# Optimization experiments

Measured on AMD Instinct MI355X. Metric: run time of the kernel, lower is better.

Reference implementation:

```python
import jax, jax.numpy as jnp
import numpy as np

B, C, H, W = 8, 256, 128, 128
NH, WS = 8, 8
HD = C // NH
WNH, WNW = H // WS, W // WS


def _rel_pos_index():
    coords = np.stack(np.meshgrid(np.arange(WS), np.arange(WS), indexing='ij'))  # [2,ws,ws]
    flat = coords.reshape(2, -1)
    rel = (flat[:, :, None] - flat[:, None, :]).transpose(1, 2, 0)  # [ws^2,ws^2,2]
    rel[..., 0] += WS - 1
    rel[..., 1] += WS - 1
    rel[..., 0] *= 2 * WS - 1
    return jnp.asarray(rel.sum(-1))  # [ws^2,ws^2]


def grid_sample(img, grid):
    # Bilinear, padding_mode='zeros', align_corners=True. img [N,C,H,W], grid [N,Hg,Wg,2] (x,y in [-1,1])
    N, Ci, Hi, Wi = img.shape
    gx = (grid[..., 0] + 1.0) * 0.5 * (Wi - 1)
    gy = (grid[..., 1] + 1.0) * 0.5 * (Hi - 1)
    x0 = jnp.floor(gx)
    y0 = jnp.floor(gy)
    x0i = x0.astype(jnp.int32)
    y0i = y0.astype(jnp.int32)
    wx1 = gx - x0
    wx0 = 1.0 - wx1
    wy1 = gy - y0
    wy0 = 1.0 - wy1
    nb = jnp.arange(N)[:, None, None]

    def corner(yi, xi, wgt):
        valid = (yi >= 0) & (yi < Hi) & (xi >= 0) & (xi < Wi)
        yc = jnp.clip(yi, 0, Hi - 1)
        xc = jnp.clip(xi, 0, Wi - 1)
        val = img[nb, :, yc, xc]  # [N,Hg,Wg,C]
        return val * (wgt * valid)[..., None]

    out = (corner(y0i, x0i, wy0 * wx0) + corner(y0i, x0i + 1, wy0 * wx1)
           + corner(y0i + 1, x0i, wy1 * wx0) + corner(y0i + 1, x0i + 1, wy1 * wx1))
    return jnp.transpose(out, (0, 3, 1, 2))


def setup_inputs() -> dict:
    key = jax.random.key(0)
    ks = jax.random.split(key, 10)
    f = lambda k, s, sc=1.0: jax.random.normal(k, s, dtype=jnp.float32) * sc
    return {
        'x': f(ks[0], (B, C, H, W)),
        'qkv_w': f(ks[1], (3 * C, C), 0.02),
        'qkv_b': f(ks[2], (3 * C,), 0.02),
        'bias_w': f(ks[3], (2 * NH, C), 0.02),
        'bias_b': f(ks[4], (2 * NH,), 0.02),
        'scale_w': f(ks[5], (2 * NH, C), 0.02),
        'scale_b': f(ks[6], (2 * NH,), 0.02),
        'proj_w': f(ks[7], (C, C), 0.02),
        'proj_b': f(ks[8], (C,), 0.02),
        'rpb_table': f(ks[9], ((2 * WS - 1) ** 2, NH), 0.02),
    }


def reference(x, qkv_w, qkv_b, bias_w, bias_b, scale_w, scale_b, proj_w, proj_b, rpb_table):
    scale = HD ** -0.5
    N = B * NH
    # ---- deterministic base sampling coordinates (shift=0, no padding since H,W % WS == 0) ----
    lin_w = jnp.linspace(-1.0, 1.0, W)
    lin_h = jnp.linspace(-1.0, 1.0, H)
    winref_w = lin_w.reshape(WNW, WS).mean(-1)  # window centers along width
    winref_h = lin_h.reshape(WNH, WS).mean(-1)
    off_w = jnp.arange(WS) * 2.0 / (W - 1)
    off_w = off_w - off_w.mean()
    off_h = jnp.arange(WS) * 2.0 / (H - 1)
    off_h = off_h - off_h.mean()
    base_x = jnp.broadcast_to(winref_w[None, None, :, None] + off_w[None, None, None, :], (WNH, WS, WNW, WS))
    base_y = jnp.broadcast_to((winref_h[:, None] + off_h[None, :])[:, :, None, None], (WNH, WS, WNW, WS))
    # ---- predicted per-head per-window biases & scales ----
    xp = jax.nn.leaky_relu(x.reshape(B, C, WNH, WS, WNW, WS).mean((3, 5)))  # [B,C,WNH,WNW]
    biases = (jnp.einsum('oc,bchw->bohw', bias_w, xp) + bias_b[None, :, None, None]).reshape(N, 2, WNH, WNW)
    bx = biases[:, 0] / WNW  # sampling_biases[:,0] / (w // ws)
    by = biases[:, 1] / WNH
    scales = (jnp.einsum('oc,bchw->bohw', scale_w, xp) + scale_b[None, :, None, None]).reshape(N, 2, WNH, WNW)
    sx, sy = scales[:, 0], scales[:, 1]
    # final = base + local_offsets * scale + bias (broadcast [N,WNH,1,WNW,1] over window interior)
    cx = base_x[None] + off_w[None, None, None, None, :] * sx[:, :, None, :, None] + bx[:, :, None, :, None]
    cy = base_y[None] + off_h[None, None, :, None, None] * sy[:, :, None, :, None] + by[:, :, None, :, None]
    grid = jnp.stack([cx, cy], -1).reshape(N, H, W, 2)
    # ---- qkv via 1x1 conv ----
    qkv = (jnp.einsum('oc,bchw->bohw', qkv_w, x) + qkv_b[None, :, None, None]).reshape(B, 3, NH, HD, H, W)
    q = qkv[:, 0].reshape(N, HD, H, W)
    k = qkv[:, 1].reshape(N, HD, H, W)
    v = qkv[:, 2].reshape(N, HD, H, W)
    ksamp = grid_sample(k, grid)
    vsamp = grid_sample(v, grid)

    def win(t):  # [N,HD,H,W] -> [B, nWin, NH, WS*WS, HD]
        t = t.reshape(B, NH, HD, WNH, WS, WNW, WS)
        return jnp.transpose(t, (0, 3, 5, 1, 4, 6, 2)).reshape(B, WNH * WNW, NH, WS * WS, HD)

    qw, kw, vw = win(q), win(ksamp), win(vsamp)
    rpb = jnp.transpose(rpb_table[_rel_pos_index().reshape(-1)].reshape(WS * WS, WS * WS, NH), (2, 0, 1))
    attn = jnp.einsum('bwhqd,bwhkd->bwhqk', qw, kw) * scale + rpb[None, None]
    attn = jax.nn.softmax(attn, axis=-1)
    out = jnp.einsum('bwhqk,bwhkd->bwhqd', attn, vw)
    out = out.reshape(B, WNH, WNW, NH, WS, WS, HD)
    out = jnp.transpose(out, (0, 3, 6, 1, 4, 2, 5)).reshape(B, C, H, W)
    out = jnp.einsum('oc,bchw->bohw', proj_w, out) + proj_b[None, :, None, None]
    return out
```

## Files before the change

### kernel.cpp

```cpp
#include <hip/hip_runtime.h>
#include <hip/hip_fp16.h>

#define B_ 8
#define C_ 256
#define H_ 128
#define W_ 128
#define NH_ 8
#define WS_ 8
#define HD_ 32
#define WN_ 16
#define NWIN_ 256
#define HW_ 16384

typedef unsigned short ushort_t;
typedef unsigned int uint_t;
typedef __attribute__((ext_vector_type(8))) short short8;
typedef _Float16 __attribute__((ext_vector_type(8))) half8;
typedef __attribute__((ext_vector_type(4))) float f32x4;

__device__ __forceinline__ ushort_t bf16_rtn(float x) {
    uint_t u = __float_as_uint(x);
    return (ushort_t)((u + 0x7FFFu + ((u >> 16) & 1u)) >> 16);
}
__device__ __forceinline__ uint_t bfpack(float a, float b) {
    return (uint_t)bf16_rtn(a) | ((uint_t)bf16_rtn(b) << 16);
}
__device__ __forceinline__ uint_t h2pack(float a, float b) {
    __half2 h = __floats2half2_rn(a, b);
    return __builtin_bit_cast(uint_t, h);
}

__global__ __launch_bounds__(256) void wpack_kernel(const float* __restrict__ w,
                            ushort_t* __restrict__ wpk) {
    int u = blockIdx.x*256 + threadIdx.x;
    int lane = u & 63;
    int f    = (u >> 6) & 3;
    int kk   = (u >> 8) & 1;
    int ks   = (u >> 9) & 3;
    int wm   = (u >> 11) & 1;
    int oc   = u >> 12;
    int o = oc*128 + wm*64 + f*16 + (lane & 15);
    int c = ks*64 + kk*32 + (lane >> 4)*8;
    const float* src = w + (size_t)o*256 + c;
    float4 v0 = *(const float4*)src;
    float4 v1 = *(const float4*)(src + 4);
    uint4 Hv;
    Hv.x = h2pack(v0.x, v0.y); Hv.y = h2pack(v0.z, v0.w);
    Hv.z = h2pack(v1.x, v1.y); Hv.w = h2pack(v1.z, v1.w);
    ((uint4*)wpk)[u] = Hv;
}

__global__ __launch_bounds__(256) void wconv_kernel(const float* __restrict__ w,
                            ushort_t* __restrict__ wh, int n4) {
    int i = blockIdx.x*256 + threadIdx.x;
    if (i >= n4) return;
    float4 v = ((const float4*)w)[i];
    ((uint2*)wh)[i] = make_uint2(bfpack(v.x, v.y), bfpack(v.z, v.w));
}

__global__ __launch_bounds__(256) void rpb_expand_kernel(const float* __restrict__ rpb_table,
                            float* __restrict__ rpbT) {
    int nh = blockIdx.x;
    int t = threadIdx.x;
    #pragma unroll
    for (int rr = 0; rr < 16; ++rr) {
        int e = t*16 + rr;
        int kcol = e >> 6, qrow = e & 63;
        int yq = qrow >> 3, xq = qrow & 7, yk = kcol >> 3, xk = kcol & 7;
        int idx = (yq - yk + 7)*15 + (xq - xk + 7);
        rpbT[((size_t)nh*64 + kcol)*64 + qrow] = rpb_table[idx*8 + nh];
    }
}

__global__ __launch_bounds__(256) void pool2_kernel(const float* __restrict__ xpart, float* __restrict__ xp) {
    int bc = blockIdx.x;
    int t = threadIdx.x;
    int wy = t >> 4, wxg = t & 15;
    const float* src = xpart + (size_t)bc*2048;
    float s = 0.f;
    #pragma unroll
    for (int i = 0; i < 8; ++i) s += src[(wy*8+i)*16 + wxg];
    s *= (1.f/64.f);
    xp[(size_t)bc*256 + t] = s > 0.f ? s : 0.01f*s;
}

__global__ __launch_bounds__(256) void params_kernel(const float* __restrict__ xp,
                              const float* __restrict__ bias_w, const float* __restrict__ bias_b,
                              const float* __restrict__ scale_w, const float* __restrict__ scale_b,
                              float* __restrict__ params) {
    __shared__ float xs[256];
    int blk = blockIdx.x;
    int b = blk >> 8, win = blk & 255;
    int t = threadIdx.x;
    xs[t] = xp[((size_t)(b*256 + t))*256 + win];
    __syncthreads();
    if (t < 32) {
        int which = t >> 4;
        int o = t & 15;
        const float* Wm = which ? scale_w : bias_w;
        float acc = which ? scale_b[o] : bias_b[o];
        for (int c = 0; c < 256; ++c) acc += Wm[o*256 + c] * xs[c];
        int nh = o >> 1, comp = o & 1;
        int n = b*8 + nh;
        float v = which ? acc : 3.96875f * acc;
        params[((size_t)(n*256 + win))*4 + which*2 + comp] = v;
    }
}

__global__ __launch_bounds__(256) void mgemm_qkvf_kernel(const ushort_t* __restrict__ wpk,
                            const float* __restrict__ x,
                            const float* __restrict__ bias,
                            ushort_t* __restrict__ qt, ushort_t* __restrict__ kv,
                            float* __restrict__ xpart) {
    __shared__ __align__(16) float Btile[64*129];
    int bid = blockIdx.x;
    int orig = (bid & 7) * 384 + (bid >> 3);
    int ocg = orig % 3;
    int rest = orig / 3;
    int hrow = rest & 127;
    int zb = rest >> 7;
    int p0 = hrow * 128;
    const float* xb = x + (size_t)zb*C_*HW_;
    ushort_t* qtb = qt + (size_t)zb*HW_*256;
    ushort_t* kvb = kv + (size_t)zb*8*HW_*64;
    int t = threadIdx.x;
    int lane = t & 63, wid = t >> 6;
    int wm = wid >> 1, wn = wid & 1;
    int qi = lane >> 4, rl = lane & 15;

    const ushort_t* wpkA0 = wpk + (size_t)((ocg*2 + 0)*2 + wm)*16384;
    const ushort_t* wpkA1 = wpk + (size_t)((ocg*2 + 1)*2 + wm)*16384;

    f32x4 acc[2][4][4];
    #pragma unroll
    for (int o2 = 0; o2 < 2; ++o2)
        #pragma unroll
        for (int f = 0; f < 4; ++f)
            #pragma unroll
            for (int g = 0; g < 4; ++g)
                acc[o2][f][g] = (f32x4){0.f, 0.f, 0.f, 0.f};

    for (int ks = 0; ks < 4; ++ks) {
        int c0 = ks*64;
        __syncthreads();
        #pragma unroll
        for (int r = 0; r < 8; ++r) {
            int task = t + r*256;
            int cl = task >> 5, p4 = (task & 31)*4;
            float4 v = *(const float4*)(xb + (size_t)(c0+cl)*HW_ + p0 + p4);
            float* dst = &Btile[cl*129 + p4];
            dst[0]=v.x; dst[1]=v.y; dst[2]=v.z; dst[3]=v.w;
        }
        __syncthreads();
        if (ocg == 0) {
            #pragma unroll
            for (int r = 0; r < 4; ++r) {
                int task = t + r*256;
                int cl = task >> 4, wxg = task & 15;
                float s = 0.f;
                #pragma unroll
                for (int j = 0; j < 8; ++j) s += Btile[cl*129 + wxg*8 + j];
                xpart[(((size_t)zb*256 + c0+cl)*128 + hrow)*16 + wxg] = s;
            }
        }
        #pragma unroll
        for (int kk = 0; kk < 2; ++kk) {
            half8 bfh[4];
            #pragma unroll
            for (int g = 0; g < 4; ++g) {
                int pix = wn*64 + g*16 + rl;
                const float* col = &Btile[(kk*32 + qi*8)*129 + pix];
                float f0 = col[0*129], f1 = col[1*129], f2 = col[2*129], f3 = col[3*129];
                float f4 = col[4*129], f5 = col[5*129], f6 = col[6*129], f7 = col[7*129];
                uint4 bu;
                bu.x = h2pack(f0, f1); bu.y = h2pack(f2, f3);
                bu.z = h2pack(f4, f5); bu.w = h2pack(f6, f7);
                bfh[g] = __builtin_bit_cast(half8, bu);
            }
            int wkoff = ((ks*2 + kk)*4)*512 + lane*8;
            {
                half8 afh[4];
                const ushort_t* wk = wpkA0 + wkoff;
                #pragma unroll
                for (int f = 0; f < 4; ++f)
                    afh[f] = *(const half8*)(wk + f*512);
                #pragma unroll
                for (int f = 0; f < 4; ++f)
                    #pragma unroll
                    for (int g = 0; g < 4; ++g)
                        acc[0][f][g] = __builtin_amdgcn_mfma_f32_16x16x32_f16(afh[f], bfh[g], acc[0][f][g], 0, 0, 0);
            }
            {
                half8 afh[4];
                const ushort_t* wk = wpkA1 + wkoff;
                #pragma unroll
                for (int f = 0; f < 4; ++f)
                    afh[f] = *(const half8*)(wk + f*512);
                #pragma unroll
                for (int f = 0; f < 4; ++f)
                    #pragma unroll
                    for (int g = 0; g < 4; ++g)
                        acc[1][f][g] = __builtin_amdgcn_mfma_f32_16x16x32_f16(afh[f], bfh[g], acc[1][f][g], 0, 0, 0);
            }
        }
    }

    float* tb = Btile;
    #pragma unroll
    for (int o2 = 0; o2 < 2; ++o2) {
        int o0 = ocg*256 + o2*128;
        #pragma unroll
        for (int pm = 0; pm < 2; ++pm) {
            #pragma unroll
            for (int pn = 0; pn < 2; ++pn) {
                __syncthreads();
                if (wm == pm && wn == pn) {
                    #pragma unroll
                    for (int f = 0; f < 4; ++f)
                        #pragma unroll
                        for (int g = 0; g < 4; ++g)
                            #pragma unroll
                            for (int r = 0; r < 4; ++r)
                                tb[(f*16 + qi*4 + r)*67 + g*16 + rl] = acc[o2][f][g][r];
                }
                __syncthreads();
                {
                    int pxl = t >> 2, cg = t & 3;
                    size_t pix = p0 + pn*64 + pxl;
                    int obase = o0 + pm*64 + cg*16;
                    int type = obase >> 8;
                    int oo = obase & 255;
                    int head = oo >> 5;
                    ushort_t* dst = (type == 0)
                        ? qtb + pix*256 + oo
                        : kvb + ((size_t)head*HW_ + pix)*64 + ((type == 2) ? 32 : 0) + (oo & 31);
                    float v[16];
                    #pragma unroll
                    for (int e = 0; e < 16; ++e) v[e] = tb[(cg*16 + e)*67 + pxl];
                    float4 b0 = *(const float4*)&bias[obase];
                    float4 b1 = *(const float4*)&bias[obase + 4];
                    float4 b2 = *(const float4*)&bias[obase + 8];
                    float4 b3 = *(const float4*)&bias[obase + 12];
                    uint4 H0, H1;
                    H0.x = h2pack(v[0]+b0.x,  v[1]+b0.y);  H0.y = h2pack(v[2]+b0.z,  v[3]+b0.w);
                    H0.z = h2pack(v[4]+b1.x,  v[5]+b1.y);  H0.w = h2pack(v[6]+b1.z,  v[7]+b1.w);
                    H1.x = h2pack(v[8]+b2.x,  v[9]+b2.y);  H1.y = h2pack(v[10]+b2.z, v[11]+b2.w);
                    H1.z = h2pack(v[12]+b3.x, v[13]+b3.y); H1.w = h2pack(v[14]+b3.z, v[15]+b3.w);
                    *(uint4*)dst = H0;
                    *(uint4*)(dst + 8) = H1;
                }
            }
        }
    }
}

__global__ __launch_bounds__(256) void mgemm_proj_kernel(const ushort_t* __restrict__ wp,
                            const ushort_t* __restrict__ at,
                            const float* __restrict__ bias, float* __restrict__ out) {
    __shared__ __align__(16) uint4 smem[2048];
    uint4* Ah = smem; uint4* Bh = smem + 1024;
    int bid = blockIdx.x;
    int orig = (bid & 7) * 256 + (bid >> 3);
    int o0 = (orig % 2) * 128;
    int rest = orig / 2;
    int p0 = (rest & 127) * 128;
    int zb = rest >> 7;
    const ushort_t* xh = at + (size_t)zb*HW_*256;
    float* outb = out + (size_t)zb*C_*HW_;
    int t = threadIdx.x;
    int lane = t & 63, wid = t >> 6;
    int wm = wid >> 1, wn = wid & 1;
    int q = lane >> 4, rl = lane & 15;

    f32x4 acc[4][4];
    #pragma unroll
    for (int f = 0; f < 4; ++f)
        #pragma unroll
        for (int g = 0; g < 4; ++g)
            acc[f][g] = (f32x4){0.f, 0.f, 0.f, 0.f};

    int srow = t >> 1, shalf = t & 1;
    int sw = srow & 7;

    for (int ks = 0; ks < 4; ++ks) {
        int c0 = ks * 64;
        __syncthreads();
        {
            const uint4* a_h = (const uint4*)(wp + (size_t)(o0+srow)*256 + c0);
            const uint4* b_h = (const uint4*)(xh + (size_t)(p0+srow)*256 + c0);
            #pragma unroll
            for (int jj = 0; jj < 4; ++jj) {
                int u = shalf*4 + jj;
                int d = srow*8 + (u ^ sw);
                Ah[d] = a_h[u]; Bh[d] = b_h[u];
            }
        }
        __syncthreads();
        #pragma unroll
        for (int kk = 0; kk < 2; ++kk) {
            short8 afh[4], bfh[4];
            #pragma unroll
            for (int f = 0; f < 4; ++f) {
                int row = wm*64 + f*16 + rl;
                int u = (kk*4 + q) ^ (row & 7);
                afh[f] = __builtin_bit_cast(short8, Ah[row*8 + u]);
            }
            #pragma unroll
            for (int g = 0; g < 4; ++g) {
                int row = wn*64 + g*16 + rl;
                int u = (kk*4 + q) ^ (row & 7);
                bfh[g] = __builtin_bit_cast(short8, Bh[row*8 + u]);
            }
            #pragma unroll
            for (int f = 0; f < 4; ++f)
                #pragma unroll
                for (int g = 0; g < 4; ++g)
                    acc[f][g] = __builtin_amdgcn_mfma_f32_16x16x32_bf16(afh[f], bfh[g], acc[f][g], 0, 0, 0);
        }
    }
    #pragma unroll
    for (int f = 0; f < 4; ++f) {
        float4 bb = *(const float4*)&bias[o0 + wm*64 + f*16 + q*4];
        float bbv[4] = {bb.x, bb.y, bb.z, bb.w};
        #pragma unroll
        for (int g = 0; g < 4; ++g) {
            int p = p0 + wn*64 + g*16 + rl;
            #pragma unroll
            for (int r = 0; r < 4; ++r) {
                int o = o0 + wm*64 + f*16 + q*4 + r;
                outb[(size_t)o*HW_ + p] = acc[f][g][r] + bbv[r];
            }
        }
    }
}

__global__ __launch_bounds__(256) void attn_kernel(const ushort_t* __restrict__ qt,
                            const ushort_t* __restrict__ kv,
                            const float* __restrict__ params_,
                            const float* __restrict__ rpbT,
                            ushort_t* __restrict__ at) {
    __shared__ __align__(16) ushort_t smem[64*40 + 64*40 + 32*72 + 64*40];
    ushort_t (*Q_lds)[40]   = (ushort_t(*)[40])smem;
    ushort_t (*K_lds)[40]   = (ushort_t(*)[40])(smem + 2560);
    ushort_t (*VT_lds)[72]  = (ushort_t(*)[72])(smem + 5120);
    ushort_t (*P_lds)[72]   = (ushort_t(*)[72])smem;
    ushort_t (*OUT_lds)[40] = (ushort_t(*)[40])(smem + 5120 + 2304);

    int b = blockIdx.y;
    int blk = blockIdx.x;
    int win = blk >> 3, nh = blk & 7;
    int wy = win >> 4, wx = win & 15;
    int t = threadIdx.x;
    int lane = t & 63, wid = t >> 6;

    const float* pp = params_ + ((size_t)((b*8 + nh)*256 + win))*4;
    float ox = pp[0], oy = pp[1], sx = pp[2], sy = pp[3];

    const ushort_t* qtb = qt + (size_t)b*HW_*256;
    const ushort_t* kvb = kv + ((size_t)(b*8 + nh))*HW_*64;
    ushort_t* ath = at + (size_t)b*HW_*256;

    {
        int tok = t >> 2, cg = t & 3;
        int i = tok >> 3, j = tok & 7;
        size_t pix = (size_t)(wy*8 + i)*W_ + wx*8 + j;
        *(uint4*)&Q_lds[tok][cg*8] = *(const uint4*)(qtb + pix*256 + nh*32 + cg*8);
    }
    {
        int tokq = lane >> 3, sub = lane & 7;
        #pragma unroll
        for (int r = 0; r < 2; ++r) {
            int tok = wid*16 + r*8 + tokq;
            int i = tok >> 3, j = tok & 7;
            int h = wy*8 + i, wpx = wx*8 + j;
            float gx = (float)wpx + ((float)j - 3.5f)*sx + ox;
            float gy = (float)h  + ((float)i - 3.5f)*sy + oy;
            float x0f = floorf(gx), y0f = floorf(gy);
            int x0 = (int)x0f, y0 = (int)y0f;
            float wx1 = gx - x0f, wy1 = gy - y0f;
            float wxz = 1.f - wx1, wyz = 1.f - wy1;
            int x1 = x0 + 1, y1 = y0 + 1;
            float m00 = wyz*wxz * ((y0>=0 && y0<H_ && x0>=0 && x0<W_) ? 1.f : 0.f);
            float m01 = wyz*wx1 * ((y0>=0 && y0<H_ && x1>=0 && x1<W_) ? 1.f : 0.f);
            float m10 = wy1*wxz * ((y1>=0 && y1<H_ && x0>=0 && x0<W_) ? 1.f : 0.f);
            float m11 = wy1*wx1 * ((y1>=0 && y1<H_ && x1>=0 && x1<W_) ? 1.f : 0.f);
            int x0c = min(max(x0,0),W_-1), x1c = min(max(x1,0),W_-1);
            int y0c = min(max(y0,0),H_-1), y1c = min(max(y1,0),H_-1);
            size_t p00 = (size_t)y0c*W_ + x0c, p01 = (size_t)y0c*W_ + x1c;
            size_t p10 = (size_t)y1c*W_ + x0c, p11 = (size_t)y1c*W_ + x1c;
            __half2 a0 = __float2half2_rn(0.f), a1 = a0, a2 = a0, a3 = a0;
            #define CORNER(PIX, M) { \
                uint4 u = *(const uint4*)(kvb + (PIX)*64 + sub*8); \
                __half2 wv = __float2half2_rn(M); \
                a0 = __hfma2(__builtin_bit_cast(__half2, u.x), wv, a0); \
                a1 = __hfma2(__builtin_bit_cast(__half2, u.y), wv, a1); \
                a2 = __hfma2(__builtin_bit_cast(__half2, u.z), wv, a2); \
                a3 = __hfma2(__builtin_bit_cast(__half2, u.w), wv, a3); }
            CORNER(p00, m00)
            CORNER(p01, m01)
            CORNER(p10, m10)
            CORNER(p11, m11)
            #undef CORNER
            if (sub < 4) {
                uint4 Kv;
                Kv.x = __builtin_bit_cast(uint_t, a0); Kv.y = __builtin_bit_cast(uint_t, a1);
                Kv.z = __builtin_bit_cast(uint_t, a2); Kv.w = __builtin_bit_cast(uint_t, a3);
                *(uint4*)&K_lds[tok][sub*8] = Kv;
            } else {
                int d0 = (sub - 4)*8;
                VT_lds[d0+0][tok] = __half_as_ushort(__low2half(a0));
                VT_lds[d0+1][tok] = __half_as_ushort(__high2half(a0));
                VT_lds[d0+2][tok] = __half_as_ushort(__low2half(a1));
                VT_lds[d0+3][tok] = __half_as_ushort(__high2half(a1));
                VT_lds[d0+4][tok] = __half_as_ushort(__low2half(a2));
                VT_lds[d0+5][tok] = __half_as_ushort(__high2half(a2));
                VT_lds[d0+6][tok] = __half_as_ushort(__low2half(a3));
                VT_lds[d0+7][tok] = __half_as_ushort(__high2half(a3));
            }
        }
    }
    __syncthreads();

    int q = lane >> 4, rl = lane & 15;
    const float scale = 0.17677669529663687f;

    half8 a_frag = *(const half8*)&Q_lds[wid*16 + rl][q*8];
    half8 b_frag[4];
    #pragma unroll
    for (int g = 0; g < 4; ++g)
        b_frag[g] = *(const half8*)&K_lds[g*16 + rl][q*8];
    __syncthreads();

    f32x4 accS[4];
    #pragma unroll
    for (int g = 0; g < 4; ++g)
        accS[g] = __builtin_amdgcn_mfma_f32_16x16x32_f16(a_frag, b_frag[g], (f32x4){0.f,0.f,0.f,0.f}, 0, 0, 0);

    float Sv[4][4];
    const float* rpbb = rpbT + (size_t)nh*4096;
    int m0 = wid*16 + q*4;
    #pragma unroll
    for (int g = 0; g < 4; ++g) {
        float4 rv = *(const float4*)&rpbb[(g*16 + rl)*64 + m0];
        Sv[g][0] = accS[g][0]*scale + rv.x;
        Sv[g][1] = accS[g][1]*scale + rv.y;
        Sv[g][2] = accS[g][2]*scale + rv.z;
        Sv[g][3] = accS[g][3]*scale + rv.w;
    }
    float inv[4];
    #pragma unroll
    for (int r = 0; r < 4; ++r) {
        float pm = fmaxf(fmaxf(Sv[0][r], Sv[1][r]), fmaxf(Sv[2][r], Sv[3][r]));
        pm = fmaxf(pm, __shfl_xor(pm, 1));
        pm = fmaxf(pm, __shfl_xor(pm, 2));
        pm = fmaxf(pm, __shfl_xor(pm, 4));
        pm = fmaxf(pm, __shfl_xor(pm, 8));
        float s = 0.f;
        #pragma unroll
        for (int g = 0; g < 4; ++g) {
            float e = __expf(Sv[g][r] - pm);
            Sv[g][r] = e;
            s += e;
        }
        s += __shfl_xor(s, 1);
        s += __shfl_xor(s, 2);
        s += __shfl_xor(s, 4);
        s += __shfl_xor(s, 8);
        inv[r] = 1.f / s;
    }
    #pragma unroll
    for (int r = 0; r < 4; ++r) {
        int m = wid*16 + q*4 + r;
        #pragma unroll
        for (int g = 0; g < 4; ++g)
            P_lds[m][g*16 + rl] = __half_as_ushort(__float2half(Sv[g][r]*inv[r]));
    }

    f32x4 accO[2] = {(f32x4){0.f,0.f,0.f,0.f}, (f32x4){0.f,0.f,0.f,0.f}};
    #pragma unroll
    for (int ks = 0; ks < 2; ++ks) {
        half8 p_frag = *(const half8*)&P_lds[wid*16 + rl][ks*32 + q*8];
        #pragma unroll
        for (int g2 = 0; g2 < 2; ++g2) {
            half8 v_frag = *(const half8*)&VT_lds[g2*16 + rl][ks*32 + q*8];
            accO[g2] = __builtin_amdgcn_mfma_f32_16x16x32_f16(p_frag, v_frag, accO[g2], 0, 0, 0);
        }
    }
    #pragma unroll
    for (int r = 0; r < 4; ++r) {
        int m = wid*16 + q*4 + r;
        OUT_lds[m][rl]      = bf16_rtn(accO[0][r]);
        OUT_lds[m][16 + rl] = bf16_rtn(accO[1][r]);
    }
    __syncthreads();
    {
        int tok = t >> 2, cg = t & 3;
        int i2 = tok >> 3, j2 = tok & 7;
        size_t pix = (size_t)(wy*8 + i2)*W_ + wx*8 + j2;
        *(uint4*)(ath + pix*256 + nh*32 + cg*8) = *(const uint4*)&OUT_lds[tok][cg*8];
    }
}

extern "C" void kernel_launch(void* const* d_in, const int* in_sizes, int n_in,
                              void* d_out, int out_size, void* d_ws, size_t ws_size,
                              hipStream_t stream) {
    const float* x       = (const float*)d_in[0];
    const float* qkv_w   = (const float*)d_in[1];
    const float* qkv_b   = (const float*)d_in[2];
    const float* bias_w  = (const float*)d_in[3];
    const float* bias_b  = (const float*)d_in[4];
    const float* scale_w = (const float*)d_in[5];
    const float* scale_b = (const float*)d_in[6];
    const float* proj_w  = (const float*)d_in[7];
    const float* proj_b  = (const float*)d_in[8];
    const float* rpb     = (const float*)d_in[9];
    float* out = (float*)d_out;

    char* ws = (char*)d_ws;
    float*    xp       = (float*)ws;     ws += (size_t)524288*4;
    float*    params   = (float*)ws;     ws += (size_t)65536*4;
    float*    xpart    = (float*)ws;     ws += (size_t)4194304*4;
    float*    rpbT     = (float*)ws;     ws += (size_t)8*4096*4;
    ushort_t* wpk      = (ushort_t*)ws;  ws += (size_t)768*256*2;
    ushort_t* wp       = (ushort_t*)ws;  ws += (size_t)256*256*2;
    ushort_t* at       = (ushort_t*)ws;  ws += (size_t)B_*HW_*256*2;
    ushort_t* qt       = (ushort_t*)ws;  ws += (size_t)B_*HW_*256*2;
    ushort_t* kv       = (ushort_t*)ws;

    wpack_kernel<<<dim3(96), 256, 0, stream>>>(qkv_w, wpk);
    wconv_kernel<<<dim3(64), 256, 0, stream>>>(proj_w, wp, 256*256/4);
    rpb_expand_kernel<<<dim3(NH_), 256, 0, stream>>>(rpb, rpbT);
    mgemm_qkvf_kernel<<<dim3(3072), 256, 0, stream>>>(wpk, x, qkv_b, qt, kv, xpart);
    pool2_kernel <<<dim3(B_*C_), 256, 0, stream>>>(xpart, xp);
    params_kernel<<<dim3(B_*NWIN_), 256, 0, stream>>>(xp, bias_w, bias_b, scale_w, scale_b, params);
    attn_kernel<<<dim3(NH_*NWIN_, B_), 256, 0, stream>>>(qt, kv, params, rpbT, at);
    mgemm_proj_kernel<<<dim3(2048), 256, 0, stream>>>(wp, at, proj_b, out);
}
```

Before: 322.3 us.

## Merge prep kernels, stage proj epilogue through LDS, remap attention block order

Folds the three small weight/rpb preparation kernels into one launch to cut launch overhead. The projection GEMM epilogue now writes each 64x64 quadrant into a padded LDS tile and stores it as coalesced float4 rows, replacing scattered scalar global stores. The attention grid becomes 1D with an XCD-aware swizzle that remaps block ids to (batch, head, window), aiming for better L2 locality across chiplets. The staged epilogue adds four serialized sync rounds per block and extra LDS use.

```diff
diff --git a/kernel.cpp b/kernel.cpp
--- a/kernel.cpp
+++ b/kernel.cpp
@@ -30,45 +30,43 @@
     return __builtin_bit_cast(uint_t, h);
 }
 
-__global__ __launch_bounds__(256) void wpack_kernel(const float* __restrict__ w,
-                            ushort_t* __restrict__ wpk) {
-    int u = blockIdx.x*256 + threadIdx.x;
-    int lane = u & 63;
-    int f    = (u >> 6) & 3;
-    int kk   = (u >> 8) & 1;
-    int ks   = (u >> 9) & 3;
-    int wm   = (u >> 11) & 1;
-    int oc   = u >> 12;
-    int o = oc*128 + wm*64 + f*16 + (lane & 15);
-    int c = ks*64 + kk*32 + (lane >> 4)*8;
-    const float* src = w + (size_t)o*256 + c;
-    float4 v0 = *(const float4*)src;
-    float4 v1 = *(const float4*)(src + 4);
-    uint4 Hv;
-    Hv.x = h2pack(v0.x, v0.y); Hv.y = h2pack(v0.z, v0.w);
-    Hv.z = h2pack(v1.x, v1.y); Hv.w = h2pack(v1.z, v1.w);
-    ((uint4*)wpk)[u] = Hv;
-}
-
-__global__ __launch_bounds__(256) void wconv_kernel(const float* __restrict__ w,
-                            ushort_t* __restrict__ wh, int n4) {
-    int i = blockIdx.x*256 + threadIdx.x;
-    if (i >= n4) return;
-    float4 v = ((const float4*)w)[i];
-    ((uint2*)wh)[i] = make_uint2(bfpack(v.x, v.y), bfpack(v.z, v.w));
-}
-
-__global__ __launch_bounds__(256) void rpb_expand_kernel(const float* __restrict__ rpb_table,
-                            float* __restrict__ rpbT) {
-    int nh = blockIdx.x;
+__global__ __launch_bounds__(256) void prep_kernel(const float* __restrict__ qkv_w,
+                            ushort_t* __restrict__ wpk,
+                            const float* __restrict__ proj_w, ushort_t* __restrict__ wp,
+                            const float* __restrict__ rpb_table, float* __restrict__ rpbT) {
+    int blk = blockIdx.x;
     int t = threadIdx.x;
-    #pragma unroll
-    for (int rr = 0; rr < 16; ++rr) {
-        int e = t*16 + rr;
-        int kcol = e >> 6, qrow = e & 63;
-        int yq = qrow >> 3, xq = qrow & 7, yk = kcol >> 3, xk = kcol & 7;
-        int idx = (yq - yk + 7)*15 + (xq - xk + 7);
-        rpbT[((size_t)nh*64 + kcol)*64 + qrow] = rpb_table[idx*8 + nh];
+    if (blk < 96) {
+        int u = blk*256 + t;
+        int lane = u & 63;
+        int f    = (u >> 6) & 3;
+        int kk   = (u >> 8) & 1;
+        int ks   = (u >> 9) & 3;
+        int wm   = (u >> 11) & 1;
+        int oc   = u >> 12;
+        int o = oc*128 + wm*64 + f*16 + (lane & 15);
+        int c = ks*64 + kk*32 + (lane >> 4)*8;
+        const float* src = qkv_w + (size_t)o*256 + c;
+        float4 v0 = *(const float4*)src;
+        float4 v1 = *(const float4*)(src + 4);
+        uint4 Hv;
+        Hv.x = h2pack(v0.x, v0.y); Hv.y = h2pack(v0.z, v0.w);
+        Hv.z = h2pack(v1.x, v1.y); Hv.w = h2pack(v1.z, v1.w);
+        ((uint4*)wpk)[u] = Hv;
+    } else if (blk < 160) {
+        int i = (blk - 96)*256 + t;
+        float4 v = ((const float4*)proj_w)[i];
+        ((uint2*)wp)[i] = make_uint2(bfpack(v.x, v.y), bfpack(v.z, v.w));
+    } else {
+        int nh = blk - 160;
+        #pragma unroll
+        for (int rr = 0; rr < 16; ++rr) {
+            int e = t*16 + rr;
+            int kcol = e >> 6, qrow = e & 63;
+            int yq = qrow >> 3, xq = qrow & 7, yk = kcol >> 3, xk = kcol & 7;
+            int idx = (yq - yk + 7)*15 + (xq - xk + 7);
+            rpbT[((size_t)nh*64 + kcol)*64 + qrow] = rpb_table[idx*8 + nh];
+        }
     }
 }
 
@@ -257,8 +255,9 @@
 __global__ __launch_bounds__(256) void mgemm_proj_kernel(const ushort_t* __restrict__ wp,
                             const ushort_t* __restrict__ at,
                             const float* __restrict__ bias, float* __restrict__ out) {
-    __shared__ __align__(16) uint4 smem[2048];
+    __shared__ __align__(16) uint4 smem[2080];
     uint4* Ah = smem; uint4* Bh = smem + 1024;
+    float* tb = (float*)smem;
     int bid = blockIdx.x;
     int orig = (bid & 7) * 256 + (bid >> 3);
     int o0 = (orig % 2) * 128;
@@ -319,16 +318,31 @@
         }
     }
     #pragma unroll
-    for (int f = 0; f < 4; ++f) {
-        float4 bb = *(const float4*)&bias[o0 + wm*64 + f*16 + q*4];
-        float bbv[4] = {bb.x, bb.y, bb.z, bb.w};
-        #pragma unroll
-        for (int g = 0; g < 4; ++g) {
-            int p = p0 + wn*64 + g*16 + rl;
-            #pragma unroll
-            for (int r = 0; r < 4; ++r) {
-                int o = o0 + wm*64 + f*16 + q*4 + r;
-                outb[(size_t)o*HW_ + p] = acc[f][g][r] + bbv[r];
+    for (int pm = 0; pm < 2; ++pm) {
+        #pragma unroll
+        for (int pn = 0; pn < 2; ++pn) {
+            __syncthreads();
+            if (wm == pm && wn == pn) {
+                #pragma unroll
+                for (int f = 0; f < 4; ++f) {
+                    float4 bb = *(const float4*)&bias[o0 + pm*64 + f*16 + q*4];
+                    float bbv[4] = {bb.x, bb.y, bb.z, bb.w};
+                    #pragma unroll
+                    for (int g = 0; g < 4; ++g)
+                        #pragma unroll
+                        for (int r = 0; r < 4; ++r)
+                            tb[(f*16 + q*4 + r)*65 + g*16 + rl] = acc[f][g][r] + bbv[r];
+                }
+            }
+            __syncthreads();
+            {
+                #pragma unroll
+                for (int r2 = 0; r2 < 4; ++r2) {
+                    int row = r2*16 + (t >> 4);
+                    int px = (t & 15) * 4;
+                    float4 v = *(const float4*)&tb[row*65 + px];
+                    *(float4*)(outb + (size_t)(o0 + pm*64 + row)*HW_ + p0 + pn*64 + px) = v;
+                }
             }
         }
     }
@@ -346,9 +360,11 @@
     ushort_t (*P_lds)[72]   = (ushort_t(*)[72])smem;
     ushort_t (*OUT_lds)[40] = (ushort_t(*)[40])(smem + 5120 + 2304);
 
-    int b = blockIdx.y;
-    int blk = blockIdx.x;
-    int win = blk >> 3, nh = blk & 7;
+    int bid = blockIdx.x;
+    int orig = (bid & 7) * 2048 + (bid >> 3);
+    int b = orig >> 11;
+    int nh = (orig >> 8) & 7;
+    int win = orig & 255;
     int wy = win >> 4, wx = win & 15;
     int t = threadIdx.x;
     int lane = t & 63, wid = t >> 6;
@@ -527,12 +543,10 @@
     ushort_t* qt       = (ushort_t*)ws;  ws += (size_t)B_*HW_*256*2;
     ushort_t* kv       = (ushort_t*)ws;
 
-    wpack_kernel<<<dim3(96), 256, 0, stream>>>(qkv_w, wpk);
-    wconv_kernel<<<dim3(64), 256, 0, stream>>>(proj_w, wp, 256*256/4);
-    rpb_expand_kernel<<<dim3(NH_), 256, 0, stream>>>(rpb, rpbT);
+    prep_kernel<<<dim3(168), 256, 0, stream>>>(qkv_w, wpk, proj_w, wp, rpb, rpbT);
     mgemm_qkvf_kernel<<<dim3(3072), 256, 0, stream>>>(wpk, x, qkv_b, qt, kv, xpart);
     pool2_kernel <<<dim3(B_*C_), 256, 0, stream>>>(xpart, xp);
     params_kernel<<<dim3(B_*NWIN_), 256, 0, stream>>>(xp, bias_w, bias_b, scale_w, scale_b, params);
-    attn_kernel<<<dim3(NH_*NWIN_, B_), 256, 0, stream>>>(qt, kv, params, rpbT, at);
+    attn_kernel<<<dim3(16384), 256, 0, stream>>>(qt, kv, params, rpbT, at);
     mgemm_proj_kernel<<<dim3(2048), 256, 0, stream>>>(wp, at, proj_b, out);
 }
```

Measured after the change: 331.3 us. 1.03x slower.
